# Optimization experiments

Measured on AMD Instinct MI355X. Metric: run time of the kernel, lower is better.

Reference implementation:

```python
import jax, jax.numpy as jnp
import numpy as np

ALPHA = 0.2

def setup_inputs() -> dict:
    key = jax.random.key(0)
    k1, k2, k3, k4 = jax.random.split(key, 4)
    B, S, I, H, O = 64, 2048, 128, 512, 64
    x = jax.random.normal(k1, (B, S, I), dtype=jnp.float32)
    # weights pre-transposed: y = x @ W (torch Linear uses x @ W.T)
    Wih = jax.random.normal(k2, (I, H), dtype=jnp.float32) / np.sqrt(I)
    W_rec = jax.random.normal(k3, (H, H), dtype=jnp.float32) / np.sqrt(H)
    Who = jax.random.normal(k4, (H, O), dtype=jnp.float32) / np.sqrt(H)
    return {"x": x, "Wih": Wih, "W_rec": W_rec, "Who": Who}

def reference(x, Wih, W_rec, Who):
    B, S, _ = x.shape
    H = W_rec.shape[0]
    u = jnp.einsum('bsi,ih->bsh', x, Wih)          # input projection, done once
    u_t = jnp.transpose(u, (1, 0, 2))              # [S, B, H] for scan
    h0 = jnp.zeros((B, H), dtype=x.dtype)          # initial_state=None -> zeros

    def step(h, u_step):
        r = jnp.tanh(u_step + h @ W_rec)           # eval mode: no noise
        h_new = (1.0 - ALPHA) * h + ALPHA * r      # leaky integration
        return h_new, h_new

    _, hs = jax.lax.scan(step, h0, u_t)            # hs: [S, B, H]
    out = jnp.einsum('sbh,ho->bso', hs, Who)       # readout, batched GEMM
    return out
```

## Files before the change

### kernel.cpp

```cpp
#include <hip/hip_runtime.h>
#include <hip/hip_fp16.h>
#include <cstdint>
#include <cstddef>

typedef _Float16 f16;
typedef _Float16 f16x2 __attribute__((ext_vector_type(2)));
typedef _Float16 f16x4 __attribute__((ext_vector_type(4)));
typedef _Float16 f16x8 __attribute__((ext_vector_type(8)));
typedef int i32x4 __attribute__((ext_vector_type(4)));
typedef float f32x4 __attribute__((ext_vector_type(4)));

#define S_LEN 2048
#define BATCH 64
#define I_DIM 128
#define H_DIM 512
#define O_DIM 64

__device__ __forceinline__ float fdot2f(f16x2 a, f16x2 b, float c) {
#if __has_builtin(__builtin_amdgcn_fdot2)
    return __builtin_amdgcn_fdot2(a, b, c, false);
#else
    return c + (float)a.x * (float)b.x + (float)a.y * (float)b.y;
#endif
}

__global__ __launch_bounds__(256)
void u_gemm_kernel(const float* __restrict__ x, const float* __restrict__ Wih,
                   f16* __restrict__ u) {
    const int tid = threadIdx.x;
    const int lane = tid & 63;
    const int w = tid >> 6;
    const int li = lane & 15;
    const int g = lane >> 4;
    const size_t r0 = (size_t)blockIdx.x * 64;
    const int c0 = blockIdx.y * 128;

    __shared__ __align__(16) f16 bT[128 * 128];

#pragma unroll
    for (int i = 0; i < 64; ++i) {
        int idx = i * 256 + tid;
        int k = idx >> 7;
        int c = idx & 127;
        float v = Wih[(size_t)k * H_DIM + c0 + c];
        bT[c * 128 + (k ^ ((c & 7) << 3))] = (f16)v;
    }

    const int tr = (int)r0 + w * 16 + li;
    f16x8 a[4];
#pragma unroll
    for (int kt = 0; kt < 4; ++kt) {
        const float* xp = x + (size_t)tr * I_DIM + kt * 32 + g * 8;
        f32x4 v0 = *(const f32x4*)(xp);
        f32x4 v1 = *(const f32x4*)(xp + 4);
        f16x8 h;
        h[0] = (f16)v0[0]; h[1] = (f16)v0[1]; h[2] = (f16)v0[2]; h[3] = (f16)v0[3];
        h[4] = (f16)v1[0]; h[5] = (f16)v1[1]; h[6] = (f16)v1[2]; h[7] = (f16)v1[3];
        a[kt] = h;
    }
    __syncthreads();

    f32x4 acc[8];
#pragma unroll
    for (int n = 0; n < 8; ++n) acc[n] = (f32x4){0.f, 0.f, 0.f, 0.f};

#pragma unroll
    for (int kt = 0; kt < 4; ++kt) {
#pragma unroll
        for (int n = 0; n < 8; ++n) {
            const int c = n * 16 + li;
            const int koff = (kt * 32 + g * 8) ^ ((c & 7) << 3);
            f16x8 b = *(const f16x8*)(&bT[c * 128 + koff]);
            acc[n] = __builtin_amdgcn_mfma_f32_16x16x32_f16(a[kt], b, acc[n], 0, 0, 0);
        }
    }

#pragma unroll
    for (int n = 0; n < 8; ++n) {
#pragma unroll
        for (int r = 0; r < 4; ++r) {
            size_t row = r0 + w * 16 + g * 4 + r;
            u[row * H_DIM + c0 + n * 16 + li] = (f16)acc[n][r];
        }
    }
}

__global__ __launch_bounds__(512, 2)
void rnn_scan_kernel(const float* __restrict__ Wrec, f16* __restrict__ uhs) {
    const int tid = threadIdx.x;
    const int b = blockIdx.x;
    const int l = tid & 63;
    const int w = tid >> 6;
    const int grp = l >> 4;
    const int li = l & 15;

    __shared__ __align__(16) signed char h8[2][512];
    __shared__ float colmax[512];

    {
        const float* wp = Wrec + tid;
        float m0 = 0.f, m1 = 0.f, m2 = 0.f, m3 = 0.f;
        for (int k = 0; k < 512; k += 4) {
            m0 = fmaxf(m0, __builtin_fabsf(wp[(size_t)(k + 0) * H_DIM]));
            m1 = fmaxf(m1, __builtin_fabsf(wp[(size_t)(k + 1) * H_DIM]));
            m2 = fmaxf(m2, __builtin_fabsf(wp[(size_t)(k + 2) * H_DIM]));
            m3 = fmaxf(m3, __builtin_fabsf(wp[(size_t)(k + 3) * H_DIM]));
        }
        float m = fmaxf(fmaxf(m0, m1), fmaxf(m2, m3));
        colmax[tid] = fmaxf(m, 1e-20f);
    }
    h8[0][tid] = 0;
    __syncthreads();

    i32x4 wf[8][4];
#pragma unroll
    for (int j = 0; j < 4; ++j) {
        const int col = w * 64 + j * 16 + li;
        const float* wp = Wrec + col;
        const float sc = 127.f / colmax[col];
#pragma unroll
        for (int kt = 0; kt < 8; ++kt) {
            int wd0 = 0, wd1 = 0, wd2 = 0, wd3 = 0;
#pragma unroll
            for (int jj = 0; jj < 16; ++jj) {
                float v = wp[(size_t)(kt * 64 + grp * 16 + jj) * H_DIM] * sc;
                v = fminf(fmaxf(v, -127.f), 127.f);
                int q = ((int)rintf(v)) & 255;
                int sh = 8 * (jj & 3);
                if (jj < 4)       wd0 |= q << sh;
                else if (jj < 8)  wd1 |= q << sh;
                else if (jj < 12) wd2 |= q << sh;
                else              wd3 |= q << sh;
            }
            i32x4 f; f.x = wd0; f.y = wd1; f.z = wd2; f.w = wd3;
            wf[kt][j] = f;
        }
    }

    f16* io = uhs + (size_t)b * S_LEN * H_DIM + tid;
    const float inv = colmax[tid] * (1.f / 16129.f);

    float hp = 0.f;
    float uc = (float)io[0];
    f16 ua = (f16)0.f;
    if (S_LEN > 1) ua = io[H_DIM];

    __syncthreads();

    for (int t = 0; t < S_LEN; ++t) {
        f16 ub = (f16)0.f;
        if (t + 2 < S_LEN) ub = io[(size_t)(t + 2) * H_DIM];

        const signed char* hb = h8[t & 1];
        i32x4 av[8];
#pragma unroll
        for (int kt = 0; kt < 8; ++kt)
            av[kt] = *(const i32x4*)(hb + kt * 64 + grp * 16);

        i32x4 a0 = {0,0,0,0}, a1 = {0,0,0,0}, a2 = {0,0,0,0}, a3 = {0,0,0,0};
#pragma unroll
        for (int kt = 0; kt < 8; ++kt) {
            a0 = __builtin_amdgcn_mfma_i32_16x16x64_i8(av[kt], wf[kt][0], a0, 0, 0, 0);
            a1 = __builtin_amdgcn_mfma_i32_16x16x64_i8(av[kt], wf[kt][1], a1, 0, 0, 0);
            a2 = __builtin_amdgcn_mfma_i32_16x16x64_i8(av[kt], wf[kt][2], a2, 0, 0, 0);
            a3 = __builtin_amdgcn_mfma_i32_16x16x64_i8(av[kt], wf[kt][3], a3, 0, 0, 0);
        }

        int zi = grp == 0 ? a0[0] : grp == 1 ? a1[0] : grp == 2 ? a2[0] : a3[0];
        float z = (float)zi * inv + uc;

        float e2 = __expf(2.f * z);
        float r = 1.f - 2.f * __builtin_amdgcn_rcpf(e2 + 1.f);
        hp = 0.8f * hp + 0.2f * r;

        h8[(t + 1) & 1][tid] = (signed char)(int)rintf(hp * 127.f);
        io[(size_t)t * H_DIM] = (f16)hp;

        uc = (float)ua;
        ua = ub;
        __syncthreads();
    }
}

__global__ __launch_bounds__(256)
void out_gemm_kernel(const f16* __restrict__ hs, const float* __restrict__ Who,
                     float* __restrict__ out) {
    const int tid = threadIdx.x;
    const int r0 = blockIdx.x * 32;

    __shared__ __align__(16) f16x2 who_s[128][O_DIM];
    __shared__ __align__(16) f16x2 hs_s[32][128];

    const int o = tid & 63;
    const int rg = tid >> 6;

    float acc[8];
#pragma unroll
    for (int r = 0; r < 8; ++r) acc[r] = 0.f;

    for (int kc = 0; kc < 2; ++kc) {
        if (kc) __syncthreads();
#pragma unroll
        for (int i = 0; i < 32; ++i) {
            int idx = i * 256 + tid;
            int kp = idx >> 6;
            int oc = idx & 63;
            float w0 = Who[(size_t)(kc * 256 + 2 * kp + 0) * O_DIM + oc];
            float w1 = Who[(size_t)(kc * 256 + 2 * kp + 1) * O_DIM + oc];
            f16x2 wv2; wv2.x = (f16)w0; wv2.y = (f16)w1;
            who_s[kp][oc] = wv2;
        }
        f16x8* hd = (f16x8*)hs_s;
#pragma unroll
        for (int i = 0; i < 4; ++i) {
            int idx = i * 256 + tid;
            int r = idx >> 5;
            int m = idx & 31;
            f16x8 v = *(const f16x8*)(hs + (size_t)(r0 + r) * H_DIM + kc * 256 + m * 8);
            hd[idx] = v;
        }
        __syncthreads();

#pragma unroll
        for (int sc = 0; sc < 4; ++sc) {
            f16x2 wv[32];
#pragma unroll
            for (int i = 0; i < 32; ++i) wv[i] = who_s[sc * 32 + i][o];
#pragma unroll
            for (int r = 0; r < 8; ++r) {
                const int row = rg * 8 + r;
#pragma unroll
                for (int m = 0; m < 8; ++m) {
                    f16x8 h8v = *(const f16x8*)(&hs_s[row][sc * 32 + 4 * m]);
                    const f16x2* hp = (const f16x2*)&h8v;
                    acc[r] = fdot2f(wv[4 * m + 0], hp[0], acc[r]);
                    acc[r] = fdot2f(wv[4 * m + 1], hp[1], acc[r]);
                    acc[r] = fdot2f(wv[4 * m + 2], hp[2], acc[r]);
                    acc[r] = fdot2f(wv[4 * m + 3], hp[3], acc[r]);
                }
            }
        }
    }
#pragma unroll
    for (int r = 0; r < 8; ++r) {
        int row = r0 + rg * 8 + r;
        out[(size_t)row * O_DIM + o] = acc[r];
    }
}

extern "C" void kernel_launch(void* const* d_in, const int* in_sizes, int n_in,
                              void* d_out, int out_size, void* d_ws, size_t ws_size,
                              hipStream_t stream) {
    const float* x    = (const float*)d_in[0];
    const float* Wih  = (const float*)d_in[1];
    const float* Wrec = (const float*)d_in[2];
    const float* Who  = (const float*)d_in[3];
    float* out = (float*)d_out;
    f16* uhs = (f16*)d_ws;

    const int R = BATCH * S_LEN;

    u_gemm_kernel<<<dim3(R / 64, H_DIM / 128), 256, 0, stream>>>(x, Wih, uhs);
    rnn_scan_kernel<<<dim3(BATCH), 512, 0, stream>>>(Wrec, uhs);
    out_gemm_kernel<<<dim3(R / 32), 256, 0, stream>>>(uhs, Who, out);
}
```

Measured before the change: 1.761 ms.

## Use MFMA for readout GEMM and defer hidden-state stores in scan

The readout GEMM moves from scalar fdot2 accumulation to f16 MFMA 16x16x32 instructions. Who is staged once into a swizzled transposed LDS tile of 64x512, and each block now covers 64 rows with A fragments loaded directly from global memory. In the recurrent scan, each step's f16 hidden-state store is deferred by one iteration, so the global write is issued at the start of the next step rather than just before the barrier. The scan is the likely bottleneck, so the readout change may matter little overall. Re-staging the full Who into LDS in every block adds per-block setup cost.

```diff
diff --git a/kernel.cpp b/kernel.cpp
--- a/kernel.cpp
+++ b/kernel.cpp
@@ -15,14 +15,6 @@
 #define I_DIM 128
 #define H_DIM 512
 #define O_DIM 64
-
-__device__ __forceinline__ float fdot2f(f16x2 a, f16x2 b, float c) {
-#if __has_builtin(__builtin_amdgcn_fdot2)
-    return __builtin_amdgcn_fdot2(a, b, c, false);
-#else
-    return c + (float)a.x * (float)b.x + (float)a.y * (float)b.y;
-#endif
-}
 
 __global__ __launch_bounds__(256)
 void u_gemm_kernel(const float* __restrict__ x, const float* __restrict__ Wih,
@@ -141,6 +133,7 @@
     const float inv = colmax[tid] * (1.f / 16129.f);
 
     float hp = 0.f;
+    f16 hh_prev = (f16)0.f;
     float uc = (float)io[0];
     f16 ua = (f16)0.f;
     if (S_LEN > 1) ua = io[H_DIM];
@@ -148,6 +141,8 @@
     __syncthreads();
 
     for (int t = 0; t < S_LEN; ++t) {
+        if (t > 0) io[(size_t)(t - 1) * H_DIM] = hh_prev;
+
         f16 ub = (f16)0.f;
         if (t + 2 < S_LEN) ub = io[(size_t)(t + 2) * H_DIM];
 
@@ -172,79 +167,67 @@
         float e2 = __expf(2.f * z);
         float r = 1.f - 2.f * __builtin_amdgcn_rcpf(e2 + 1.f);
         hp = 0.8f * hp + 0.2f * r;
+        f16 hh = (f16)hp;
 
         h8[(t + 1) & 1][tid] = (signed char)(int)rintf(hp * 127.f);
-        io[(size_t)t * H_DIM] = (f16)hp;
+        hh_prev = hh;
 
         uc = (float)ua;
         ua = ub;
         __syncthreads();
     }
+    io[(size_t)(S_LEN - 1) * H_DIM] = hh_prev;
 }
 
 __global__ __launch_bounds__(256)
 void out_gemm_kernel(const f16* __restrict__ hs, const float* __restrict__ Who,
                      float* __restrict__ out) {
     const int tid = threadIdx.x;
-    const int r0 = blockIdx.x * 32;
-
-    __shared__ __align__(16) f16x2 who_s[128][O_DIM];
-    __shared__ __align__(16) f16x2 hs_s[32][128];
-
-    const int o = tid & 63;
-    const int rg = tid >> 6;
-
-    float acc[8];
-#pragma unroll
-    for (int r = 0; r < 8; ++r) acc[r] = 0.f;
-
-    for (int kc = 0; kc < 2; ++kc) {
-        if (kc) __syncthreads();
-#pragma unroll
-        for (int i = 0; i < 32; ++i) {
-            int idx = i * 256 + tid;
-            int kp = idx >> 6;
-            int oc = idx & 63;
-            float w0 = Who[(size_t)(kc * 256 + 2 * kp + 0) * O_DIM + oc];
-            float w1 = Who[(size_t)(kc * 256 + 2 * kp + 1) * O_DIM + oc];
-            f16x2 wv2; wv2.x = (f16)w0; wv2.y = (f16)w1;
-            who_s[kp][oc] = wv2;
-        }
-        f16x8* hd = (f16x8*)hs_s;
-#pragma unroll
-        for (int i = 0; i < 4; ++i) {
-            int idx = i * 256 + tid;
-            int r = idx >> 5;
-            int m = idx & 31;
-            f16x8 v = *(const f16x8*)(hs + (size_t)(r0 + r) * H_DIM + kc * 256 + m * 8);
-            hd[idx] = v;
-        }
-        __syncthreads();
-
-#pragma unroll
-        for (int sc = 0; sc < 4; ++sc) {
-            f16x2 wv[32];
-#pragma unroll
-            for (int i = 0; i < 32; ++i) wv[i] = who_s[sc * 32 + i][o];
-#pragma unroll
-            for (int r = 0; r < 8; ++r) {
-                const int row = rg * 8 + r;
-#pragma unroll
-                for (int m = 0; m < 8; ++m) {
-                    f16x8 h8v = *(const f16x8*)(&hs_s[row][sc * 32 + 4 * m]);
-                    const f16x2* hp = (const f16x2*)&h8v;
-                    acc[r] = fdot2f(wv[4 * m + 0], hp[0], acc[r]);
-                    acc[r] = fdot2f(wv[4 * m + 1], hp[1], acc[r]);
-                    acc[r] = fdot2f(wv[4 * m + 2], hp[2], acc[r]);
-                    acc[r] = fdot2f(wv[4 * m + 3], hp[3], acc[r]);
-                }
-            }
-        }
-    }
-#pragma unroll
-    for (int r = 0; r < 8; ++r) {
-        int row = r0 + rg * 8 + r;
-        out[(size_t)row * O_DIM + o] = acc[r];
+    const int lane = tid & 63;
+    const int w = tid >> 6;
+    const int li = lane & 15;
+    const int g = lane >> 4;
+    const size_t r0 = (size_t)blockIdx.x * 64;
+
+    __shared__ __align__(16) f16 bT[64 * 512];
+
+#pragma unroll 4
+    for (int i = 0; i < 128; ++i) {
+        int idx = i * 256 + tid;
+        int k = idx >> 6;
+        int c = idx & 63;
+        float v = Who[(size_t)k * O_DIM + c];
+        bT[c * 512 + (k ^ ((c & 7) << 3))] = (f16)v;
+    }
+
+    const size_t tr = r0 + w * 16 + li;
+    const f16* ap = hs + tr * H_DIM + g * 8;
+
+    __syncthreads();
+
+    f32x4 acc[4];
+#pragma unroll
+    for (int n = 0; n < 4; ++n) acc[n] = (f32x4){0.f, 0.f, 0.f, 0.f};
+
+#pragma unroll
+    for (int kt = 0; kt < 16; ++kt) {
+        f16x8 a = *(const f16x8*)(ap + kt * 32);
+#pragma unroll
+        for (int n = 0; n < 4; ++n) {
+            const int c = n * 16 + li;
+            const int koff = (kt * 32 + g * 8) ^ ((c & 7) << 3);
+            f16x8 b = *(const f16x8*)(&bT[c * 512 + koff]);
+            acc[n] = __builtin_amdgcn_mfma_f32_16x16x32_f16(a, b, acc[n], 0, 0, 0);
+        }
+    }
+
+#pragma unroll
+    for (int n = 0; n < 4; ++n) {
+#pragma unroll
+        for (int r = 0; r < 4; ++r) {
+            size_t row = r0 + w * 16 + g * 4 + r;
+            out[row * O_DIM + n * 16 + li] = acc[n][r];
+        }
     }
 }
 
@@ -262,5 +245,5 @@
 
     u_gemm_kernel<<<dim3(R / 64, H_DIM / 128), 256, 0, stream>>>(x, Wih, uhs);
     rnn_scan_kernel<<<dim3(BATCH), 512, 0, stream>>>(Wrec, uhs);
-    out_gemm_kernel<<<dim3(R / 32), 256, 0, stream>>>(uhs, Who, out);
-}
+    out_gemm_kernel<<<dim3(R / 64), 256, 0, stream>>>(uhs, Who, out);
+}
```

After: 1.670 ms. 1.05x faster.
